# Kernel tuning notes

Hardware: AMD Instinct MI355X
Metric: run time of the kernel (lower is better)

## Reference

```python
import jax, jax.numpy as jnp
import numpy as np

N = 100000
E = 3200000
F_IN = 27
H1, C1 = 8, 8
H2, C2 = 1, 2
NEG_SLOPE = 0.2


def gat_conv(x, src, dst, W, a_src, a_dst, b, heads, ch, n_nodes):
    # x: [N, F_in]; src/dst: [E'] (self-loops already appended)
    h = (x @ W).reshape(n_nodes, heads, ch)            # [N, H, C]
    alpha_src = jnp.sum(h * a_src, axis=-1)            # [N, H]
    alpha_dst = jnp.sum(h * a_dst, axis=-1)            # [N, H]
    e = jax.nn.leaky_relu(alpha_src[src] + alpha_dst[dst], NEG_SLOPE)  # [E', H]
    m = jax.ops.segment_max(e, dst, num_segments=n_nodes)             # [N, H]
    ex = jnp.exp(e - m[dst])
    denom = jax.ops.segment_sum(ex, dst, num_segments=n_nodes)        # [N, H]
    alpha = ex / denom[dst]                                           # [E', H]
    out = jax.ops.segment_sum(h[src] * alpha[:, :, None], dst, num_segments=n_nodes)
    return out.reshape(n_nodes, heads * ch) + b


def setup_inputs() -> dict:
    key = jax.random.key(0)
    ks = jax.random.split(key, 10)
    x = jax.random.normal(ks[0], (N, F_IN), dtype=jnp.float32)
    edge_index = jax.random.randint(ks[1], (2, E), 0, N, dtype=jnp.int64)
    s1 = 1.0 / np.sqrt(F_IN)
    s2 = 1.0 / np.sqrt(H1 * C1)
    W1 = jax.random.uniform(ks[2], (F_IN, H1 * C1), jnp.float32, -s1, s1)
    a_src1 = jax.random.uniform(ks[3], (H1, C1), jnp.float32, -s1, s1)
    a_dst1 = jax.random.uniform(ks[4], (H1, C1), jnp.float32, -s1, s1)
    b1 = jnp.zeros((H1 * C1,), jnp.float32)
    W2 = jax.random.uniform(ks[5], (H1 * C1, H2 * C2), jnp.float32, -s2, s2)
    a_src2 = jax.random.uniform(ks[6], (H2, C2), jnp.float32, -s2, s2)
    a_dst2 = jax.random.uniform(ks[7], (H2, C2), jnp.float32, -s2, s2)
    b2 = jnp.zeros((H2 * C2,), jnp.float32)
    return {"x": x, "edge_index": edge_index, "W1": W1, "a_src1": a_src1,
            "a_dst1": a_dst1, "b1": b1, "W2": W2, "a_src2": a_src2,
            "a_dst2": a_dst2, "b2": b2}


def reference(x, edge_index, W1, a_src1, a_dst1, b1, W2, a_src2, a_dst2, b2):
    # eval mode: dropouts are identity. PyG GATConv adds self-loops by default.
    loop = jnp.arange(N, dtype=edge_index.dtype)
    src = jnp.concatenate([edge_index[0], loop])
    dst = jnp.concatenate([edge_index[1], loop])
    h = jax.nn.elu(gat_conv(x, src, dst, W1, a_src1, a_dst1, b1, H1, C1, N))
    out = gat_conv(h, src, dst, W2, a_src2, a_dst2, b2, H2, C2, N)
    return jax.nn.log_softmax(out, axis=1)
```

## Files before the change

### kernel.cpp

```cpp
#include <hip/hip_runtime.h>
#include <hip/hip_fp16.h>
#include <math.h>

#define NN 100000
#define EE 3200000
#define ET (EE + NN)

#define H1n 8
#define C1n 8
#define F1n 64
#define FINn 27
#define NEG 0.2f

#define NPB 128
#define NB 782
#define STRIDE 5120
#define TILE 4096
#define ABLK 256
#define EPT (TILE / ABLK)
#define WIN (STRIDE + NPB)
#define FBLK 512
#define RPT 10

typedef float floatx2 __attribute__((ext_vector_type(2)));

static __device__ __forceinline__ float lrelu(float v) {
    return v > 0.f ? v : NEG * v;
}

__global__ __launch_bounds__(ABLK) void k_binA(const int* __restrict__ ei,
                                               int* __restrict__ tail,
                                               int* __restrict__ recs) {
    __shared__ int hist[NB];
    __shared__ int lofs[NB];
    __shared__ int wofs[NB];
    __shared__ int sorted[TILE];
    __shared__ unsigned short sbkt[TILE];
    __shared__ int wls[ABLK / 64];

    int tid = threadIdx.x;
    long long e0 = (long long)blockIdx.x * TILE;
    int cnt = (int)min((long long)TILE, (long long)EE - e0);

    for (int i = tid; i < NB; i += ABLK) hist[i] = 0;
    __syncthreads();

    int ss[EPT], dd[EPT], rk[EPT];
    #pragma unroll
    for (int k = 0; k < EPT; ++k) {
        int idx = k * ABLK + tid;
        if (idx < cnt) {
            ss[k] = ei[e0 + idx];
            dd[k] = ei[EE + e0 + idx];
            rk[k] = atomicAdd(&hist[dd[k] >> 7], 1);
        }
    }
    __syncthreads();
    {
        const int CH = (NB + ABLK - 1) / ABLK;
        int beg = tid * CH, end = min(beg + CH, NB);
        int s = 0;
        for (int i = beg; i < end; ++i) s += hist[i];
        int lane = tid & 63, wv = tid >> 6;
        int inc = s;
        #pragma unroll
        for (int off = 1; off < 64; off <<= 1) {
            int t = __shfl_up(inc, off, 64);
            if (lane >= off) inc += t;
        }
        if (lane == 63) wls[wv] = inc;
        __syncthreads();
        int pre = 0;
        #pragma unroll
        for (int w = 0; w < ABLK / 64; ++w) pre += (w < wv) ? wls[w] : 0;
        int ex = pre + inc - s;
        for (int i = beg; i < end; ++i) {
            lofs[i] = ex;
            ex += hist[i];
        }
    }
    __syncthreads();
    #pragma unroll
    for (int k = 0; k < EPT; ++k) {
        int idx = k * ABLK + tid;
        if (idx < cnt) {
            int b = dd[k] >> 7;
            int r = lofs[b] + rk[k];
            sorted[r] = ss[k] | ((dd[k] & (NPB - 1)) << 17);
            sbkt[r] = (unsigned short)b;
        }
    }
    __syncthreads();
    for (int i = tid; i < NB; i += ABLK) {
        int c = hist[i];
        int g = (c > 0) ? atomicAdd(&tail[i], c) : 0;
        wofs[i] = g - lofs[i];
    }
    __syncthreads();
    for (int t = tid; t < cnt; t += ABLK) {
        int b = sbkt[t];
        recs[(size_t)b * STRIDE + wofs[b] + t] = sorted[t];
    }
}

__global__ __launch_bounds__(256) void k_h1(const float* __restrict__ x,
                                            const float* __restrict__ W1,
                                            const float* __restrict__ a_src1,
                                            const float* __restrict__ a_dst1,
                                            unsigned char* __restrict__ h1q,
                                            __half* __restrict__ as1h,
                                            float* __restrict__ ad1) {
    int gt = blockIdx.x * blockDim.x + threadIdx.x;
    int n = gt >> 6;
    if (n >= NN) return;
    int lane = threadIdx.x & 63;
    const float* xr = x + (size_t)n * FINn;
    float s = 0.f;
    #pragma unroll
    for (int k = 0; k < FINn; ++k) s = fmaf(xr[k], W1[k * F1n + lane], s);
    float s2 = __shfl_down(s, 1, 64);
    if (!(lane & 1)) {
        int pk = __builtin_amdgcn_cvt_pk_fp8_f32(s, s2, 0, false);
        ((unsigned short*)(h1q + (size_t)n * F1n))[lane >> 1] =
            (unsigned short)(pk & 0xFFFF);
    }
    float ps = s * a_src1[lane];
    float pd = s * a_dst1[lane];
    #pragma unroll
    for (int off = 1; off < 8; off <<= 1) {
        ps += __shfl_xor(ps, off, 64);
        pd += __shfl_xor(pd, off, 64);
    }
    if ((lane & 7) == 0) {
        int h = lane >> 3;
        as1h[n * H1n + h] = __float2half(ps);
        ad1[n * H1n + h] = pd;
    }
}

__global__ __launch_bounds__(FBLK) void k_sort(const int* __restrict__ recs,
                                               const int* __restrict__ tail,
                                               int* __restrict__ gwin,
                                               uint2* __restrict__ nrange) {
    __shared__ int hist[NPB];
    __shared__ int cur[NPB];
    __shared__ int rloc[NPB + 1];
    __shared__ int window[WIN];
    __shared__ int wtot[2];

    int b = blockIdx.x;
    int tid = threadIdx.x;
    int node0 = b * NPB;
    int nodes = min(NPB, NN - node0);
    int rcnt = tail[b];
    const int* rb = recs + (size_t)b * STRIDE;

    if (tid < NPB) hist[tid] = 0;
    __syncthreads();
    int rg[RPT];
    int nmine = 0;
    #pragma unroll
    for (int k = 0; k < RPT; ++k) {
        int i = tid + k * FBLK;
        if (i < rcnt) {
            rg[k] = rb[i];
            atomicAdd(&hist[rg[k] >> 17], 1);
            nmine = k + 1;
        }
    }
    __syncthreads();
    int v = 0, inc = 0;
    if (tid < NPB) {
        v = (tid < nodes) ? hist[tid] + 1 : 0;
        inc = v;
        #pragma unroll
        for (int off = 1; off < 64; off <<= 1) {
            int t = __shfl_up(inc, off, 64);
            if ((tid & 63) >= off) inc += t;
        }
        if ((tid & 63) == 63) wtot[tid >> 6] = inc;
    }
    __syncthreads();
    if (tid < NPB) {
        if (tid >= 64) inc += wtot[0];
        int ex = inc - v;
        if (tid < nodes) {
            rloc[tid] = ex;
            cur[tid] = ex + 1;
            window[ex] = node0 + tid;
        }
    }
    if (tid == 0) rloc[nodes] = wtot[0] + wtot[1];
    __syncthreads();
    #pragma unroll
    for (int k = 0; k < RPT; ++k) {
        if (k < nmine) {
            int r = rg[k];
            int p = atomicAdd(&cur[r >> 17], 1);
            window[p] = r & 0x1FFFF;
        }
    }
    __syncthreads();
    int T = rloc[nodes];
    int gbase = b * WIN;
    for (int i = tid; i < T; i += FBLK)
        gwin[gbase + i] = window[i];
    if (tid < nodes) {
        uint2 r;
        r.x = (unsigned)(gbase + rloc[tid]);
        r.y = (unsigned)(gbase + rloc[tid + 1]);
        nrange[node0 + tid] = r;
    }
}

__global__ __launch_bounds__(FBLK) void k_mp(const int* __restrict__ gwin,
                                             const uint2* __restrict__ nrange,
                                             const unsigned* __restrict__ h1q,
                                             const __half* __restrict__ as1h,
                                             const float* __restrict__ ad1,
                                             const float* __restrict__ b1,
                                             const float* __restrict__ W2,
                                             const float* __restrict__ a_src2,
                                             const float* __restrict__ a_dst2,
                                             uint2* __restrict__ rec2) {
    int n = (int)(((unsigned)blockIdx.x * FBLK + threadIdx.x) >> 6);
    if (n >= NN) return;
    int lane = threadIdx.x & 63;
    int e8 = lane >> 3;
    int hh = lane & 7;
    int q = lane >> 4;
    int c4 = lane & 15;
    int bpe = e8 << 2;
    int bpq = q << 2;
    int bpx = ((q << 3) + (c4 >> 1)) << 2;

    float adh = ad1[(n << 3) + hh];
    uint2 rr = nrange[n];
    float a0 = 0.f, a1 = 0.f, a2 = 0.f, a3 = 0.f, den = 0.f;

    for (unsigned base = rr.x; base < rr.y; base += 64) {
        int cnt = (int)min(64u, rr.y - base);
        int sidx = (lane < cnt) ? gwin[base + lane] : 0;
        for (int sb = 0; sb < cnt; sb += 8) {
            int sb4 = sb << 2;
            int s_sc = __builtin_amdgcn_ds_bpermute(sb4 + bpe, sidx);
            float A = __half2float(as1h[((unsigned)s_sc << 3) + hh]);
            float sc = A + adh;
            sc = fmaxf(sc, 0.2f * sc);
            float x = (sb + e8 < cnt) ? __expf(sc) : 0.f;
            den += x;
            int xi = __float_as_int(x);
            #pragma unroll
            for (int jj = 0; jj < 2; ++jj) {
                int s_a = __builtin_amdgcn_ds_bpermute(sb4 + (jj << 4) + bpq, sidx);
                int xr_ = __builtin_amdgcn_ds_bpermute((jj << 7) + bpx, xi);
                float xv = __int_as_float(xr_);
                unsigned dw = h1q[((unsigned)s_a << 4) + c4];
                floatx2 lo = __builtin_amdgcn_cvt_pk_f32_fp8((int)dw, false);
                floatx2 hi = __builtin_amdgcn_cvt_pk_f32_fp8((int)dw, true);
                a0 = fmaf(xv, lo.x, a0);
                a1 = fmaf(xv, lo.y, a1);
                a2 = fmaf(xv, hi.x, a2);
                a3 = fmaf(xv, hi.y, a3);
            }
        }
    }

    den += __shfl_xor(den, 8, 64);
    den += __shfl_xor(den, 16, 64);
    den += __shfl_xor(den, 32, 64);
    den = __int_as_float(
        __builtin_amdgcn_ds_bpermute((c4 >> 1) << 2, __float_as_int(den)));
    #pragma unroll
    for (int off = 16; off < 64; off <<= 1) {
        a0 += __shfl_xor(a0, off, 64);
        a1 += __shfl_xor(a1, off, 64);
        a2 += __shfl_xor(a2, off, 64);
        a3 += __shfl_xor(a3, off, 64);
    }
    float inv = 1.f / den;
    float v0 = a0 * inv + b1[c4 * 4 + 0];
    float v1 = a1 * inv + b1[c4 * 4 + 1];
    float v2 = a2 * inv + b1[c4 * 4 + 2];
    float v3 = a3 * inv + b1[c4 * 4 + 3];
    v0 = v0 > 0.f ? v0 : expm1f(v0);
    v1 = v1 > 0.f ? v1 : expm1f(v1);
    v2 = v2 > 0.f ? v2 : expm1f(v2);
    v3 = v3 > 0.f ? v3 : expm1f(v3);
    float p0 = v0 * W2[(c4 * 4 + 0) * 2 + 0] + v1 * W2[(c4 * 4 + 1) * 2 + 0] +
               v2 * W2[(c4 * 4 + 2) * 2 + 0] + v3 * W2[(c4 * 4 + 3) * 2 + 0];
    float p1 = v0 * W2[(c4 * 4 + 0) * 2 + 1] + v1 * W2[(c4 * 4 + 1) * 2 + 1] +
               v2 * W2[(c4 * 4 + 2) * 2 + 1] + v3 * W2[(c4 * 4 + 3) * 2 + 1];
    #pragma unroll
    for (int off = 1; off < 16; off <<= 1) {
        p0 += __shfl_xor(p0, off, 64);
        p1 += __shfl_xor(p1, off, 64);
    }
    if (lane == 0) {
        float as2 = p0 * a_src2[0] + p1 * a_src2[1];
        float ad2 = p0 * a_dst2[0] + p1 * a_dst2[1];
        __half2 lo2 = __floats2half2_rn(p0, p1);
        __half2 hi2 = __floats2half2_rn(as2, ad2);
        uint2 r;
        r.x = *(unsigned*)&lo2;
        r.y = *(unsigned*)&hi2;
        rec2[n] = r;
    }
}

__global__ __launch_bounds__(256) void k_f2(const int* __restrict__ gwin,
                                            const uint2* __restrict__ nrange,
                                            const uint2* __restrict__ rec2,
                                            const float* __restrict__ b2,
                                            float* __restrict__ out) {
    int n = blockIdx.x * blockDim.x + threadIdx.x;
    if (n >= NN) return;
    __half2 mysd = *(const __half2*)&rec2[n].y;
    float adv = __half2float(__high2half(mysd));
    uint2 rr = nrange[n];
    float den = 0.f, a0 = 0.f, a1 = 0.f;
    for (unsigned i = rr.x; i < rr.y; ++i) {
        int s = gwin[i];
        uint2 rv = rec2[s];
        __half2 h01 = *(const __half2*)&rv.x;
        __half2 hsd = *(const __half2*)&rv.y;
        float e = lrelu(__half2float(__low2half(hsd)) + adv);
        float ex = __expf(e);
        den += ex;
        a0 = fmaf(ex, __half2float(__low2half(h01)), a0);
        a1 = fmaf(ex, __half2float(__high2half(h01)), a1);
    }
    float v0 = a0 / den + b2[0];
    float v1 = a1 / den + b2[1];
    float mx = fmaxf(v0, v1);
    float ls = mx + logf(__expf(v0 - mx) + __expf(v1 - mx));
    float2 o;
    o.x = v0 - ls;
    o.y = v1 - ls;
    ((float2*)out)[n] = o;
}

extern "C" void kernel_launch(void* const* d_in, const int* in_sizes, int n_in,
                              void* d_out, int out_size, void* d_ws, size_t ws_size,
                              hipStream_t stream) {
    const float* x      = (const float*)d_in[0];
    const int*   ei     = (const int*)d_in[1];
    const float* W1     = (const float*)d_in[2];
    const float* a_src1 = (const float*)d_in[3];
    const float* a_dst1 = (const float*)d_in[4];
    const float* b1     = (const float*)d_in[5];
    const float* W2     = (const float*)d_in[6];
    const float* a_src2 = (const float*)d_in[7];
    const float* a_dst2 = (const float*)d_in[8];
    const float* b2     = (const float*)d_in[9];
    float* out = (float*)d_out;

    char* wsb = (char*)d_ws;
    size_t o = 0;
    uint2* rec2 = (uint2*)wsb;                   o += (size_t)NN * 8;
    uint2* nrange = (uint2*)(wsb + o);           o += (size_t)NN * 8;
    #define ALLOC(name, type, count) type* name = (type*)(wsb + o); o += (size_t)(count) * 4;
    ALLOC(ad1,    float, NN * H1n)
    ALLOC(recs,   int,   (size_t)NB * STRIDE)
    ALLOC(gwin,   int,   (size_t)NB * WIN)
    ALLOC(tail,   int,   NB)
    #undef ALLOC
    __half* as1h = (__half*)(wsb + o);               o += (size_t)NN * H1n * 2;
    unsigned char* h1q = (unsigned char*)(wsb + o);  o += (size_t)NN * F1n;

    const int B = 256;
    #define GRID(n) ((unsigned)(((long long)(n) + B - 1) / B))

    hipMemsetAsync(tail, 0, (size_t)NB * sizeof(int), stream);
    k_binA<<<(EE + TILE - 1) / TILE, ABLK, 0, stream>>>(ei, tail, recs);

    k_h1<<<GRID((size_t)NN * 64), B, 0, stream>>>(x, W1, a_src1, a_dst1, h1q, as1h, ad1);

    k_sort<<<NB, FBLK, 0, stream>>>(recs, tail, gwin, nrange);

    k_mp<<<(unsigned)(((size_t)NN * 64 + FBLK - 1) / FBLK), FBLK, 0, stream>>>(
        gwin, nrange, (const unsigned*)h1q, as1h, ad1, b1, W2, a_src2, a_dst2, rec2);

    k_f2<<<GRID(NN), B, 0, stream>>>(gwin, nrange, rec2, b2, out);
    #undef GRID
}
```

Before: 211.3 us.

## Fuse layer-1 projection into edge binning kernel with vectorized edge loads

Merges the per-node feature projection kernel (k_h1) into the edge binning kernel. Each of the 782 binning blocks now also computes h1/alpha for 128 nodes after its scatter, which removes one launch and lets the projection overlap with binning work. The block size doubles to 512 threads and edge indices are read as int4 vectors. In exchange the binning kernel gets longer and heavier on registers, and the edge-to-thread assignment inside the histogram pass changes.

```diff
diff --git a/kernel.cpp b/kernel.cpp
--- a/kernel.cpp
+++ b/kernel.cpp
@@ -16,7 +16,7 @@
 #define NB 782
 #define STRIDE 5120
 #define TILE 4096
-#define ABLK 256
+#define ABLK 512
 #define EPT (TILE / ABLK)
 #define WIN (STRIDE + NPB)
 #define FBLK 512
@@ -28,9 +28,16 @@
     return v > 0.f ? v : NEG * v;
 }
 
-__global__ __launch_bounds__(ABLK) void k_binA(const int* __restrict__ ei,
-                                               int* __restrict__ tail,
-                                               int* __restrict__ recs) {
+__global__ __launch_bounds__(ABLK) void k_binA_h1(const int* __restrict__ ei,
+                                                  int* __restrict__ tail,
+                                                  int* __restrict__ recs,
+                                                  const float* __restrict__ x,
+                                                  const float* __restrict__ W1,
+                                                  const float* __restrict__ a_src1,
+                                                  const float* __restrict__ a_dst1,
+                                                  unsigned char* __restrict__ h1q,
+                                                  __half* __restrict__ as1h,
+                                                  float* __restrict__ ad1) {
     __shared__ int hist[NB];
     __shared__ int lofs[NB];
     __shared__ int wofs[NB];
@@ -39,7 +46,8 @@
     __shared__ int wls[ABLK / 64];
 
     int tid = threadIdx.x;
-    long long e0 = (long long)blockIdx.x * TILE;
+    int b = blockIdx.x;
+    long long e0 = (long long)b * TILE;
     int cnt = (int)min((long long)TILE, (long long)EE - e0);
 
     for (int i = tid; i < NB; i += ABLK) hist[i] = 0;
@@ -47,12 +55,28 @@
 
     int ss[EPT], dd[EPT], rk[EPT];
     #pragma unroll
-    for (int k = 0; k < EPT; ++k) {
-        int idx = k * ABLK + tid;
-        if (idx < cnt) {
-            ss[k] = ei[e0 + idx];
-            dd[k] = ei[EE + e0 + idx];
-            rk[k] = atomicAdd(&hist[dd[k] >> 7], 1);
+    for (int j = 0; j < EPT / 4; ++j) {
+        int idx4 = j * (ABLK * 4) + tid * 4;
+        if (idx4 + 3 < cnt) {
+            int4 sv = *(const int4*)&ei[e0 + idx4];
+            int4 dv = *(const int4*)&ei[EE + e0 + idx4];
+            ss[j * 4 + 0] = sv.x; ss[j * 4 + 1] = sv.y;
+            ss[j * 4 + 2] = sv.z; ss[j * 4 + 3] = sv.w;
+            dd[j * 4 + 0] = dv.x; dd[j * 4 + 1] = dv.y;
+            dd[j * 4 + 2] = dv.z; dd[j * 4 + 3] = dv.w;
+            #pragma unroll
+            for (int c = 0; c < 4; ++c)
+                rk[j * 4 + c] = atomicAdd(&hist[dd[j * 4 + c] >> 7], 1);
+        } else {
+            #pragma unroll
+            for (int c = 0; c < 4; ++c) {
+                int idx = idx4 + c;
+                if (idx < cnt) {
+                    ss[j * 4 + c] = ei[e0 + idx];
+                    dd[j * 4 + c] = ei[EE + e0 + idx];
+                    rk[j * 4 + c] = atomicAdd(&hist[dd[j * 4 + c] >> 7], 1);
+                }
+            }
         }
     }
     __syncthreads();
@@ -81,13 +105,17 @@
     }
     __syncthreads();
     #pragma unroll
-    for (int k = 0; k < EPT; ++k) {
-        int idx = k * ABLK + tid;
-        if (idx < cnt) {
-            int b = dd[k] >> 7;
-            int r = lofs[b] + rk[k];
-            sorted[r] = ss[k] | ((dd[k] & (NPB - 1)) << 17);
-            sbkt[r] = (unsigned short)b;
+    for (int j = 0; j < EPT / 4; ++j) {
+        #pragma unroll
+        for (int c = 0; c < 4; ++c) {
+            int k = j * 4 + c;
+            int idx = j * (ABLK * 4) + tid * 4 + c;
+            if (idx < cnt) {
+                int bb = dd[k] >> 7;
+                int r = lofs[bb] + rk[k];
+                sorted[r] = ss[k] | ((dd[k] & (NPB - 1)) << 17);
+                sbkt[r] = (unsigned short)bb;
+            }
         }
     }
     __syncthreads();
@@ -98,43 +126,41 @@
     }
     __syncthreads();
     for (int t = tid; t < cnt; t += ABLK) {
-        int b = sbkt[t];
-        recs[(size_t)b * STRIDE + wofs[b] + t] = sorted[t];
-    }
-}
-
-__global__ __launch_bounds__(256) void k_h1(const float* __restrict__ x,
-                                            const float* __restrict__ W1,
-                                            const float* __restrict__ a_src1,
-                                            const float* __restrict__ a_dst1,
-                                            unsigned char* __restrict__ h1q,
-                                            __half* __restrict__ as1h,
-                                            float* __restrict__ ad1) {
-    int gt = blockIdx.x * blockDim.x + threadIdx.x;
-    int n = gt >> 6;
-    if (n >= NN) return;
-    int lane = threadIdx.x & 63;
-    const float* xr = x + (size_t)n * FINn;
-    float s = 0.f;
-    #pragma unroll
-    for (int k = 0; k < FINn; ++k) s = fmaf(xr[k], W1[k * F1n + lane], s);
-    float s2 = __shfl_down(s, 1, 64);
-    if (!(lane & 1)) {
-        int pk = __builtin_amdgcn_cvt_pk_fp8_f32(s, s2, 0, false);
-        ((unsigned short*)(h1q + (size_t)n * F1n))[lane >> 1] =
-            (unsigned short)(pk & 0xFFFF);
-    }
-    float ps = s * a_src1[lane];
-    float pd = s * a_dst1[lane];
-    #pragma unroll
-    for (int off = 1; off < 8; off <<= 1) {
-        ps += __shfl_xor(ps, off, 64);
-        pd += __shfl_xor(pd, off, 64);
-    }
-    if ((lane & 7) == 0) {
-        int h = lane >> 3;
-        as1h[n * H1n + h] = __float2half(ps);
-        ad1[n * H1n + h] = pd;
+        int bb = sbkt[t];
+        recs[(size_t)bb * STRIDE + wofs[bb] + t] = sorted[t];
+    }
+
+    {
+        int lane = tid & 63;
+        int wv = tid >> 6;
+        float asl = a_src1[lane];
+        float adl = a_dst1[lane];
+        for (int m = 0; m < NPB / 8; ++m) {
+            int n = b * NPB + wv * (NPB / 8) + m;
+            if (n >= NN) break;
+            const float* xr = x + (size_t)n * FINn;
+            float s = 0.f;
+            #pragma unroll
+            for (int k = 0; k < FINn; ++k) s = fmaf(xr[k], W1[k * F1n + lane], s);
+            float s2 = __shfl_down(s, 1, 64);
+            if (!(lane & 1)) {
+                int pk = __builtin_amdgcn_cvt_pk_fp8_f32(s, s2, 0, false);
+                ((unsigned short*)(h1q + (size_t)n * F1n))[lane >> 1] =
+                    (unsigned short)(pk & 0xFFFF);
+            }
+            float ps = s * asl;
+            float pd = s * adl;
+            #pragma unroll
+            for (int off = 1; off < 8; off <<= 1) {
+                ps += __shfl_xor(ps, off, 64);
+                pd += __shfl_xor(pd, off, 64);
+            }
+            if ((lane & 7) == 0) {
+                int h = lane >> 3;
+                as1h[n * H1n + h] = __float2half(ps);
+                ad1[n * H1n + h] = pd;
+            }
+        }
     }
 }
 
@@ -372,9 +398,8 @@
     #define GRID(n) ((unsigned)(((long long)(n) + B - 1) / B))
 
     hipMemsetAsync(tail, 0, (size_t)NB * sizeof(int), stream);
-    k_binA<<<(EE + TILE - 1) / TILE, ABLK, 0, stream>>>(ei, tail, recs);
-
-    k_h1<<<GRID((size_t)NN * 64), B, 0, stream>>>(x, W1, a_src1, a_dst1, h1q, as1h, ad1);
+    k_binA_h1<<<(EE + TILE - 1) / TILE, ABLK, 0, stream>>>(
+        ei, tail, recs, x, W1, a_src1, a_dst1, h1q, as1h, ad1);
 
     k_sort<<<NB, FBLK, 0, stream>>>(recs, tail, gwin, nrange);
 
```

Result: no change. 210.6 us, median of 2 (-0.3%).
